# Kernel optimization log

Hardware: AMD Instinct MI355X
Metric: run time of the kernel (lower is better)

Reference implementation:

```python
import jax, jax.numpy as jnp
import numpy as np

B, NL, C, H, W = 4, 2048, 128, 128, 128
N_PTS0, N_PTS1 = 32, 8
SCALE = N_PTS0 // N_PTS1  # MaxPool1d kernel/stride
FEATURE_DIM = 5
BN_EPS = 1e-5


def setup_inputs() -> dict:
    key = jax.random.key(0)
    ks = jax.random.split(key, 12)
    fm = jax.random.normal(ks[0], (B, C, H, W), dtype=jnp.float32)
    lines = jax.random.uniform(ks[1], (B, NL, 2, 2), dtype=jnp.float32) * 128.0
    P = C // 2
    s = 0.05
    return {
        "feature_map": fm,
        "lines": lines,
        # Bottleneck1D params (BatchNorm in eval mode: running_mean=0, running_var=1)
        "bn1_g": jnp.ones((C,), jnp.float32), "bn1_b": jnp.zeros((C,), jnp.float32),
        "conv1_w": jax.random.normal(ks[2], (P, C, 1), jnp.float32) * s,
        "conv1_b": jnp.zeros((P,), jnp.float32),
        "bn2_g": jnp.ones((P,), jnp.float32), "bn2_b": jnp.zeros((P,), jnp.float32),
        "conv2_w": jax.random.normal(ks[3], (P, P, 3), jnp.float32) * s,
        "conv2_b": jnp.zeros((P,), jnp.float32),
        "bn3_g": jnp.ones((P,), jnp.float32), "bn3_b": jnp.zeros((P,), jnp.float32),
        "conv3_w": jax.random.normal(ks[4], (C, P, 1), jnp.float32) * s,
        "conv3_b": jnp.zeros((C,), jnp.float32),
        # fc2: ReLU -> Linear(dim_loi*n_pts1 + 5, 4)
        "fc2_w": jax.random.normal(ks[5], (4, C * N_PTS1 + FEATURE_DIM), jnp.float32) * s,
        "fc2_b": jnp.zeros((4,), jnp.float32),
    }


def _bn(x, g, b):
    # eval-mode BatchNorm1d with running_mean=0, running_var=1
    return x * (g / jnp.sqrt(1.0 + BN_EPS))[None, :, None] + b[None, :, None]


def _conv1d(x, w, b, pad):
    y = jax.lax.conv_general_dilated(x, w, (1,), [(pad, pad)],
                                     dimension_numbers=("NCH", "OIH", "NCH"))
    return y + b[None, :, None]


def _loi_gather(fm, lines):
    # sample points along each line: [B, NL, N_PTS0, 2]
    lam = jnp.linspace(0.0, 1.0, N_PTS0, dtype=jnp.float32)[None, None, :, None]
    p = lines[:, :, 0:1, :] * lam + lines[:, :, 1:2, :] * (1.0 - lam) - 0.5
    p = p.reshape(B, -1, 2)                      # [B, NL*N_PTS0, 2]
    px, py = p[..., 0], p[..., 1]
    px0 = jnp.clip(jnp.floor(px), 0.0, 127.0)
    py0 = jnp.clip(jnp.floor(py), 0.0, 127.0)
    px1 = jnp.clip(px0 + 1.0, 0.0, 127.0)
    py1 = jnp.clip(py0 + 1.0, 0.0, 127.0)
    px0l, py0l = px0.astype(jnp.int32), py0.astype(jnp.int32)
    px1l, py1l = px1.astype(jnp.int32), py1.astype(jnp.int32)

    gather = jax.vmap(lambda f, yi, xi: f[:, yi, xi])  # [C, P] per image
    # weights exactly as in the torch source
    xp = (gather(fm, py0l, px0l) * ((px1 - px) * (py1 - py))[:, None, :]
          + gather(fm, py1l, px0l) * ((px - px0) * (py1 - py))[:, None, :]
          + gather(fm, py0l, px1l) * ((px1 - px) * (py - py0))[:, None, :]
          + gather(fm, py1l, px1l) * ((px - px0) * (py - py0))[:, None, :])
    # [B, C, NL*N_PTS0] -> [B*NL, C, N_PTS0]
    xp = xp.reshape(B, C, NL, N_PTS0).transpose(0, 2, 1, 3).reshape(B * NL, C, N_PTS0)
    return xp


def reference(feature_map, lines, bn1_g, bn1_b, conv1_w, conv1_b,
              bn2_g, bn2_b, conv2_w, conv2_b, bn3_g, bn3_b,
              conv3_w, conv3_b, fc2_w, fc2_b):
    xp = _loi_gather(feature_map, lines)               # [B*NL, C, N_PTS0]
    # MaxPool1d(SCALE, SCALE)
    x = xp.reshape(B * NL, C, N_PTS1, SCALE).max(axis=-1)
    # Bottleneck1D residual block
    y = jax.nn.relu(_bn(x, bn1_g, bn1_b))
    y = _conv1d(y, conv1_w, conv1_b, 0)
    y = jax.nn.relu(_bn(y, bn2_g, bn2_b))
    y = _conv1d(y, conv2_w, conv2_b, 1)
    y = jax.nn.relu(_bn(y, bn3_g, bn3_b))
    y = _conv1d(y, conv3_w, conv3_b, 0)
    x = x + y                                          # [B*NL, C, N_PTS1]
    # line geometry feature (use_cood=1, use_slop=1)
    xyu, xyv = lines[:, :, 0, :], lines[:, :, 1, :]
    u2v = jnp.sqrt(((xyu - xyv) ** 2).sum(-1, keepdims=True)).clip(min=1e-6)
    f = jnp.concatenate([xyu / 128.0, xyv / 128.0, u2v], axis=-1)
    f = f.reshape(B * NL, FEATURE_DIM)
    # concat + fc2 (ReLU -> Linear)
    x = jnp.concatenate([x.reshape(B * NL, C * N_PTS1), f], axis=1)
    logits = jax.nn.relu(x) @ fc2_w.T + fc2_b
    prob = jax.nn.softmax(logits, axis=1)
    return logits, prob
```

## Files before the change

### kernel.cpp

```cpp
#include <hip/hip_runtime.h>
#include <math.h>

#define BB 4
#define NLL 2048
#define CC 128
#define HH 128
#define WW 128
#define NPTS0 32
#define NPTS1 8
#define PP 64
#define FDIM 5
#define FCK (CC*NPTS1 + FDIM)
#define FCKP 1032

typedef __attribute__((ext_vector_type(8))) short bf16x8;
typedef __attribute__((ext_vector_type(4))) float f32x4;

__device__ __forceinline__ unsigned short f2bf(float f) {
    union { float f; unsigned u; } v; v.f = f;
    unsigned u = v.u;
    return (unsigned short)((u + 0x7fffu + ((u >> 16) & 1u)) >> 16);
}
__device__ __forceinline__ float bf2f(unsigned short s) {
    union { unsigned u; float f; } v; v.u = ((unsigned)s) << 16;
    return v.f;
}

__global__ __launch_bounds__(256)
void transpose_prep(const float* __restrict__ fm, const float* __restrict__ w1,
                    const float* __restrict__ w2, const float* __restrict__ w3,
                    const float* __restrict__ fcw,
                    unsigned short* __restrict__ fmT,
                    unsigned short* __restrict__ W1b,
                    unsigned short* __restrict__ W2b,
                    unsigned short* __restrict__ W3b,
                    float* __restrict__ fcwP) {
    const int t = threadIdx.x;
    if (blockIdx.x >= 1024) {
        int gid = (blockIdx.x - 1024) * 256 + t;
        for (int e = gid; e < 32800; e += 4096) {
            if (e < 8192) {
                W1b[e] = f2bf(w1[e]);
            } else if (e < 20480) {
                int g = e - 8192;
                int tt = g >> 12, r = g & 4095;
                int p = r >> 6, q = r & 63;
                W2b[tt * 4096 + p * 64 + q] = f2bf(w2[p * 192 + q * 3 + tt]);
            } else if (e < 28672) {
                int g = e - 20480;
                W3b[g] = f2bf(w3[g]);
            } else {
                int g = e - 28672;
                int o = g / FCKP, r = g - o * FCKP;
                fcwP[g] = (r < FCK) ? fcw[o * FCK + r] : 0.0f;
            }
        }
        return;
    }
    __shared__ unsigned short tile[128 * 72];
    const int bh = blockIdx.x;
    const int by = bh >> 1;
    const int h  = bh & 1;
    const int b = by >> 7, y = by & 127;
    const float* src = fm + ((size_t)b * CC) * (HH * WW) + (size_t)y * WW + h * 64;
    const int x4 = (t & 15) * 4;
    #pragma unroll
    for (int i = 0; i < 8; ++i) {
        int r = (t >> 4) + 16 * i;
        float4 v = *(const float4*)&src[(size_t)r * (HH * WW) + x4];
        ushort4 u;
        u.x = f2bf(v.x); u.y = f2bf(v.y); u.z = f2bf(v.z); u.w = f2bf(v.w);
        *(ushort4*)&tile[r * 72 + (x4 ^ (r & 28))] = u;
    }
    __syncthreads();
    const int c4 = (t & 31) * 4;
    unsigned short* dst = fmT + ((size_t)by * WW + h * 64) * CC;
    #pragma unroll
    for (int i = 0; i < 8; ++i) {
        int x = (t >> 5) + 8 * i;
        ushort4 u;
        u.x = tile[(c4 + 0) * 72 + (x ^ ((c4 + 0) & 28))];
        u.y = tile[(c4 + 1) * 72 + (x ^ ((c4 + 1) & 28))];
        u.z = tile[(c4 + 2) * 72 + (x ^ ((c4 + 2) & 28))];
        u.w = tile[(c4 + 3) * 72 + (x ^ ((c4 + 3) & 28))];
        *(ushort4*)&dst[(size_t)x * CC + c4] = u;
    }
}

__global__ __launch_bounds__(256, 5)
void line_mfma(const unsigned short* __restrict__ fmT,
               const float* __restrict__ lines,
               const float* __restrict__ bn1_g, const float* __restrict__ bn1_b,
               const unsigned short* __restrict__ W1b, const float* __restrict__ b1,
               const float* __restrict__ bn2_g, const float* __restrict__ bn2_b,
               const unsigned short* __restrict__ W2b, const float* __restrict__ b2,
               const float* __restrict__ bn3_g, const float* __restrict__ bn3_b,
               const unsigned short* __restrict__ W3b, const float* __restrict__ b3,
               const float* __restrict__ fcwP,  const float* __restrict__ fcb,
               float* __restrict__ out) {
    __shared__ int   s_oA[64], s_oB[64], s_oC[64], s_oD[64];
    __shared__ float s_wA[64], s_wB[64], s_wC[64], s_wD[64];
    __shared__ float s_xs[16 * 132];
    __shared__ unsigned short s_ybn[16 * 136];
    __shared__ unsigned short s_z1[2 * 10 * 72];
    __shared__ unsigned short s_z2[16 * 72];
    __shared__ float s_feat[2][8];
    __shared__ float s_red[4 * 8];

    const int bx  = blockIdx.x;
    const int L0  = bx * 2;
    const int b   = bx >> 10;
    const int tid = threadIdx.x;
    const int lane = tid & 63;
    const int wv   = tid >> 6;
    const int quad = lane >> 4;
    const int l16  = lane & 15;
    const float inv_s = 1.0f / sqrtf(1.0f + 1e-5f);

    if (tid < 64) {
        int line = tid >> 5, pt = tid & 31;
        const float* ln = lines + (size_t)(L0 + line) * 4;
        float lam = (float)pt * (1.0f / 31.0f);
        float om  = 1.0f - lam;
        float px = ln[0] * lam + ln[2] * om - 0.5f;
        float py = ln[1] * lam + ln[3] * om - 0.5f;
        float px0 = fminf(fmaxf(floorf(px), 0.0f), 127.0f);
        float py0 = fminf(fmaxf(floorf(py), 0.0f), 127.0f);
        float px1 = fminf(px0 + 1.0f, 127.0f);
        float py1 = fminf(py0 + 1.0f, 127.0f);
        int ix0 = (int)px0, ix1 = (int)px1, iy0 = (int)py0, iy1 = (int)py1;
        s_oA[tid] = (iy0 * WW + ix0) * CC;
        s_oB[tid] = (iy1 * WW + ix0) * CC;
        s_oC[tid] = (iy0 * WW + ix1) * CC;
        s_oD[tid] = (iy1 * WW + ix1) * CC;
        float ax = px1 - px, bxv = px - px0, ay = py1 - py, byv = py - py0;
        s_wA[tid] = ax  * ay;
        s_wB[tid] = bxv * ay;
        s_wC[tid] = ax  * byv;
        s_wD[tid] = bxv * byv;
    }
    if (tid >= 64 && tid < 66) {
        int line = tid - 64;
        const float* ln = lines + (size_t)(L0 + line) * 4;
        float ux = ln[0], uy = ln[1], vx = ln[2], vy = ln[3];
        float dx = ux - vx, dy = uy - vy;
        float d = fmaxf(sqrtf(dx * dx + dy * dy), 1e-6f);
        s_feat[line][0] = ux * (1.0f / 128.0f);
        s_feat[line][1] = uy * (1.0f / 128.0f);
        s_feat[line][2] = vx * (1.0f / 128.0f);
        s_feat[line][3] = vy * (1.0f / 128.0f);
        s_feat[line][4] = d;
    }
    if (tid < 128) {
        int line = tid >> 6, q = tid & 63;
        s_z1[line * 720 + 0 * 72 + q] = 0;
        s_z1[line * 720 + 9 * 72 + q] = 0;
    }
    __syncthreads();

    {
        int tl = tid >> 4;
        int line = tl >> 3, k = tl & 7;
        int c8 = (tid & 15) * 8;
        const unsigned short* base = fmT + (size_t)b * (HH * WW * CC) + c8;
        const int pt0 = line * 32 + k * 4;
        bf16x8 rA[4], rB[4], rC[4], rD[4];
        #pragma unroll
        for (int j = 0; j < 4; ++j) {
            rA[j] = *(const bf16x8*)(base + s_oA[pt0 + j]);
            rB[j] = *(const bf16x8*)(base + s_oB[pt0 + j]);
            rC[j] = *(const bf16x8*)(base + s_oC[pt0 + j]);
            rD[j] = *(const bf16x8*)(base + s_oD[pt0 + j]);
        }
        float acc[8];
        #pragma unroll
        for (int i = 0; i < 8; ++i) acc[i] = -INFINITY;
        #pragma unroll
        for (int j = 0; j < 4; ++j) {
            int pt = pt0 + j;
            float wA = s_wA[pt], wB = s_wB[pt], wC = s_wC[pt], wD = s_wD[pt];
            #pragma unroll
            for (int i = 0; i < 8; ++i) {
                float v = wA * bf2f((unsigned short)rA[j][i])
                        + wB * bf2f((unsigned short)rB[j][i])
                        + wC * bf2f((unsigned short)rC[j][i])
                        + wD * bf2f((unsigned short)rD[j][i]);
                acc[i] = fmaxf(acc[i], v);
            }
        }
        float* xr = &s_xs[tl * 132 + c8];
        f32x4 lo = {acc[0], acc[1], acc[2], acc[3]};
        f32x4 hi = {acc[4], acc[5], acc[6], acc[7]};
        *(f32x4*)&xr[0] = lo;
        *(f32x4*)&xr[4] = hi;
        bf16x8 pack;
        #pragma unroll
        for (int i = 0; i < 8; ++i) {
            float v = fmaxf(acc[i] * (bn1_g[c8 + i] * inv_s) + bn1_b[c8 + i], 0.0f);
            pack[i] = (short)f2bf(v);
        }
        *(bf16x8*)&s_ybn[tl * 136 + c8] = pack;
    }
    __syncthreads();

    {
        int n0 = wv * 16;
        f32x4 acc = {0.f, 0.f, 0.f, 0.f};
        #pragma unroll
        for (int kc = 0; kc < 4; ++kc) {
            bf16x8 a = *(const bf16x8*)&s_ybn[l16 * 136 + kc * 32 + quad * 8];
            bf16x8 bf = *(const bf16x8*)(W1b + (n0 + l16) * 128 + kc * 32 + quad * 8);
            acc = __builtin_amdgcn_mfma_f32_16x16x32_bf16(a, bf, acc, 0, 0, 0);
        }
        int p = n0 + l16;
        float s2 = bn2_g[p] * inv_s, bb2 = bn2_b[p], cb = b1[p];
        int line = quad >> 1;
        int kbase = (quad & 1) * 4;
        #pragma unroll
        for (int r = 0; r < 4; ++r) {
            float v = fmaxf((acc[r] + cb) * s2 + bb2, 0.0f);
            s_z1[line * 720 + (kbase + r + 1) * 72 + p] = f2bf(v);
        }
    }
    __syncthreads();

    {
        int n0 = wv * 16;
        f32x4 acc = {0.f, 0.f, 0.f, 0.f};
        int line = l16 >> 3, k = l16 & 7;
        #pragma unroll
        for (int t = 0; t < 3; ++t) {
            const unsigned short* arow = &s_z1[line * 720 + (k + t) * 72];
            #pragma unroll
            for (int kc = 0; kc < 2; ++kc) {
                bf16x8 a = *(const bf16x8*)&arow[kc * 32 + quad * 8];
                bf16x8 bf = *(const bf16x8*)(W2b + t * 4096 + (n0 + l16) * 64 + kc * 32 + quad * 8);
                acc = __builtin_amdgcn_mfma_f32_16x16x32_bf16(a, bf, acc, 0, 0, 0);
            }
        }
        int p = n0 + l16;
        float s3 = bn3_g[p] * inv_s, bb3 = bn3_b[p], cb = b2[p];
        #pragma unroll
        for (int r = 0; r < 4; ++r) {
            float v = fmaxf((acc[r] + cb) * s3 + bb3, 0.0f);
            s_z2[(quad * 4 + r) * 72 + p] = f2bf(v);
        }
    }
    __syncthreads();

    float p0 = 0.f, p1 = 0.f, p2 = 0.f, p3 = 0.f;
    {
        int kbase = (quad & 1) * 4;
        bf16x8 a0 = *(const bf16x8*)&s_z2[l16 * 72 + 0 * 32 + quad * 8];
        bf16x8 a1 = *(const bf16x8*)&s_z2[l16 * 72 + 1 * 32 + quad * 8];
        #pragma unroll
        for (int sub = 0; sub < 2; ++sub) {
            int n0 = wv * 32 + sub * 16;
            f32x4 acc = {0.f, 0.f, 0.f, 0.f};
            bf16x8 bf0 = *(const bf16x8*)(W3b + (n0 + l16) * 64 + 0 * 32 + quad * 8);
            bf16x8 bf1 = *(const bf16x8*)(W3b + (n0 + l16) * 64 + 1 * 32 + quad * 8);
            acc = __builtin_amdgcn_mfma_f32_16x16x32_bf16(a0, bf0, acc, 0, 0, 0);
            acc = __builtin_amdgcn_mfma_f32_16x16x32_bf16(a1, bf1, acc, 0, 0, 0);
            int c = n0 + l16;
            float cb = b3[c];
            int idx = c * 8 + kbase;
            float4 w0 = *(const float4*)(fcwP + 0 * FCKP + idx);
            float4 w1v = *(const float4*)(fcwP + 1 * FCKP + idx);
            float4 w2v = *(const float4*)(fcwP + 2 * FCKP + idx);
            float4 w3v = *(const float4*)(fcwP + 3 * FCKP + idx);
            const float* w0a = (const float*)&w0;
            const float* w1a = (const float*)&w1v;
            const float* w2a = (const float*)&w2v;
            const float* w3a = (const float*)&w3v;
            #pragma unroll
            for (int r = 0; r < 4; ++r) {
                int m = quad * 4 + r;
                float v = fmaxf(s_xs[m * 132 + c] + acc[r] + cb, 0.0f);
                p0 = fmaf(v, w0a[r], p0);
                p1 = fmaf(v, w1a[r], p1);
                p2 = fmaf(v, w2a[r], p2);
                p3 = fmaf(v, w3a[r], p3);
            }
        }
    }
    #pragma unroll
    for (int off = 16; off >= 1; off >>= 1) {
        p0 += __shfl_down(p0, off);
        p1 += __shfl_down(p1, off);
        p2 += __shfl_down(p2, off);
        p3 += __shfl_down(p3, off);
    }
    if ((lane & 31) == 0) {
        int line = lane >> 5;
        s_red[wv * 8 + line * 4 + 0] = p0;
        s_red[wv * 8 + line * 4 + 1] = p1;
        s_red[wv * 8 + line * 4 + 2] = p2;
        s_red[wv * 8 + line * 4 + 3] = p3;
    }
    __syncthreads();

    if (tid < 2) {
        int line = tid;
        float lg[4];
        #pragma unroll
        for (int o = 0; o < 4; ++o) {
            lg[o] = fcb[o] + s_red[0 + line * 4 + o] + s_red[8 + line * 4 + o]
                  + s_red[16 + line * 4 + o] + s_red[24 + line * 4 + o];
        }
        #pragma unroll
        for (int j = 0; j < FDIM; ++j) {
            float fv = fmaxf(s_feat[line][j], 0.0f);
            #pragma unroll
            for (int o = 0; o < 4; ++o)
                lg[o] = fmaf(fv, fcwP[o * FCKP + 1024 + j], lg[o]);
        }
        float m = fmaxf(fmaxf(lg[0], lg[1]), fmaxf(lg[2], lg[3]));
        float e0 = expf(lg[0] - m), e1 = expf(lg[1] - m);
        float e2 = expf(lg[2] - m), e3 = expf(lg[3] - m);
        float inv = 1.0f / (e0 + e1 + e2 + e3);
        float* lo = out + (size_t)(L0 + line) * 4;
        lo[0] = lg[0]; lo[1] = lg[1]; lo[2] = lg[2]; lo[3] = lg[3];
        float* pr = out + (size_t)BB * NLL * 4 + (size_t)(L0 + line) * 4;
        pr[0] = e0 * inv; pr[1] = e1 * inv; pr[2] = e2 * inv; pr[3] = e3 * inv;
    }
}

__global__ __launch_bounds__(256)
void transpose_fm2(const float* __restrict__ fm, float* __restrict__ fmT) {
    __shared__ float tile[32 * 132];
    const int c0 = blockIdx.x * 32;
    const int by = blockIdx.y;
    const int b = by >> 7, y = by & 127;
    const int t = threadIdx.x;
    const float* src = fm + ((size_t)b * CC) * (HH * WW) + (size_t)y * WW;
    const int x4 = (t & 31) * 4;
    #pragma unroll
    for (int i = 0; i < 4; ++i) {
        int r = (t >> 5) + 8 * i;
        *(float4*)&tile[r * 132 + x4] =
            *(const float4*)&src[(size_t)(c0 + r) * (HH * WW) + x4];
    }
    __syncthreads();
    float* dst = fmT + (size_t)by * WW * CC + c0 + (t & 31);
    const int cr = (t & 31) * 132;
    #pragma unroll
    for (int i = 0; i < 16; ++i) {
        int x = (t >> 5) + 8 * i;
        dst[(size_t)x * CC] = tile[cr + x];
    }
}

template<bool TRANS>
__global__ __launch_bounds__(256)
void line_kernel_v1(const float* __restrict__ fm,
                    const float* __restrict__ lines,
                    const float* __restrict__ bn1_g, const float* __restrict__ bn1_b,
                    const float* __restrict__ w1,    const float* __restrict__ b1,
                    const float* __restrict__ bn2_g, const float* __restrict__ bn2_b,
                    const float* __restrict__ w2,    const float* __restrict__ b2,
                    const float* __restrict__ bn3_g, const float* __restrict__ bn3_b,
                    const float* __restrict__ w3,    const float* __restrict__ b3,
                    const float* __restrict__ fcw,   const float* __restrict__ fcb,
                    float* __restrict__ out) {
    __shared__ int   s_ix0[32], s_ix1[32], s_iy0[32], s_iy1[32];
    __shared__ float s_wA[32], s_wB[32], s_wC[32], s_wD[32];
    __shared__ float xs [8][132];
    __shared__ float ybn[8][132];
    __shared__ float z1 [64][12];
    __shared__ float z2 [64][8];
    __shared__ float s_feat[8];
    __shared__ float s_red[16];

    const int L   = blockIdx.x;
    const int b   = L / NLL;
    const int tid = threadIdx.x;
    const float inv_s = 1.0f / sqrtf(1.0f + 1e-5f);
    const float* ln = lines + (size_t)L * 4;

    if (tid < 32) {
        float lam = (float)tid * (1.0f / 31.0f);
        float om  = 1.0f - lam;
        float px = ln[0] * lam + ln[2] * om - 0.5f;
        float py = ln[1] * lam + ln[3] * om - 0.5f;
        float px0 = fminf(fmaxf(floorf(px), 0.0f), 127.0f);
        float py0 = fminf(fmaxf(floorf(py), 0.0f), 127.0f);
        float px1 = fminf(px0 + 1.0f, 127.0f);
        float py1 = fminf(py0 + 1.0f, 127.0f);
        s_ix0[tid] = (int)px0; s_ix1[tid] = (int)px1;
        s_iy0[tid] = (int)py0; s_iy1[tid] = (int)py1;
        float ax = px1 - px, bxv = px - px0, ay = py1 - py, byv = py - py0;
        s_wA[tid] = ax  * ay;  s_wB[tid] = bxv * ay;
        s_wC[tid] = ax  * byv; s_wD[tid] = bxv * byv;
    }
    if (tid == 0) {
        float ux = ln[0], uy = ln[1], vx = ln[2], vy = ln[3];
        float dx = ux - vx, dy = uy - vy;
        float d = fmaxf(sqrtf(dx * dx + dy * dy), 1e-6f);
        s_feat[0] = ux / 128.0f; s_feat[1] = uy / 128.0f;
        s_feat[2] = vx / 128.0f; s_feat[3] = vy / 128.0f;
        s_feat[4] = d;
    }
    __syncthreads();
    {
        int cq = tid & 31, k = tid >> 5, c0 = cq * 4;
        float4 acc;
        acc.x = -INFINITY; acc.y = -INFINITY; acc.z = -INFINITY; acc.w = -INFINITY;
        #pragma unroll
        for (int j = 0; j < 4; ++j) {
            int pt = k * 4 + j;
            int ix0 = s_ix0[pt], ix1 = s_ix1[pt];
            int iy0 = s_iy0[pt], iy1 = s_iy1[pt];
            float wA = s_wA[pt], wB = s_wB[pt], wC = s_wC[pt], wD = s_wD[pt];
            float4 vA, vB, vC, vD;
            if (TRANS) {
                const float* base = fm + (size_t)b * HH * WW * CC;
                vA = *(const float4*)(base + ((size_t)(iy0 * WW + ix0)) * CC + c0);
                vB = *(const float4*)(base + ((size_t)(iy1 * WW + ix0)) * CC + c0);
                vC = *(const float4*)(base + ((size_t)(iy0 * WW + ix1)) * CC + c0);
                vD = *(const float4*)(base + ((size_t)(iy1 * WW + ix1)) * CC + c0);
            } else {
                const float* base = fm + ((size_t)b * CC + c0) * HH * WW;
                int oA = iy0 * WW + ix0, oB = iy1 * WW + ix0;
                int oC = iy0 * WW + ix1, oD = iy1 * WW + ix1;
                vA.x = base[oA];           vB.x = base[oB];
                vC.x = base[oC];           vD.x = base[oD];
                vA.y = base[HH*WW + oA];   vB.y = base[HH*WW + oB];
                vC.y = base[HH*WW + oC];   vD.y = base[HH*WW + oD];
                vA.z = base[2*HH*WW + oA]; vB.z = base[2*HH*WW + oB];
                vC.z = base[2*HH*WW + oC]; vD.z = base[2*HH*WW + oD];
                vA.w = base[3*HH*WW + oA]; vB.w = base[3*HH*WW + oB];
                vC.w = base[3*HH*WW + oC]; vD.w = base[3*HH*WW + oD];
            }
            float4 v;
            v.x = wA * vA.x + wB * vB.x + wC * vC.x + wD * vD.x;
            v.y = wA * vA.y + wB * vB.y + wC * vC.y + wD * vD.y;
            v.z = wA * vA.z + wB * vB.z + wC * vC.z + wD * vD.z;
            v.w = wA * vA.w + wB * vB.w + wC * vC.w + wD * vD.w;
            acc.x = fmaxf(acc.x, v.x); acc.y = fmaxf(acc.y, v.y);
            acc.z = fmaxf(acc.z, v.z); acc.w = fmaxf(acc.w, v.w);
        }
        *(float4*)(&xs[k][c0]) = acc;
    }
    __syncthreads();
    for (int e = tid; e < 1024; e += 256) {
        int k = e >> 7, c = e & 127;
        ybn[k][c] = fmaxf(xs[k][c] * (bn1_g[c] * inv_s) + bn1_b[c], 0.0f);
    }
    __syncthreads();
    if (tid < 64) { z1[tid][0] = 0.0f; z1[tid][9] = 0.0f; }
    {
        int p = tid >> 2, kq = tid & 3;
        const float* wrow = w1 + p * 128;
        float a0a = 0.f, a0b = 0.f, a1a = 0.f, a1b = 0.f;
        #pragma unroll 8
        for (int c = 0; c < 128; c += 4) {
            float4 w  = *(const float4*)(wrow + c);
            float4 ya = *(const float4*)(&ybn[kq][c]);
            float4 yb = *(const float4*)(&ybn[kq + 4][c]);
            a0a = fmaf(w.x, ya.x, a0a); a0b = fmaf(w.y, ya.y, a0b);
            a0a = fmaf(w.z, ya.z, a0a); a0b = fmaf(w.w, ya.w, a0b);
            a1a = fmaf(w.x, yb.x, a1a); a1b = fmaf(w.y, yb.y, a1b);
            a1a = fmaf(w.z, yb.z, a1a); a1b = fmaf(w.w, yb.w, a1b);
        }
        float s2 = bn2_g[p] * inv_s, bb = bn2_b[p], cb = b1[p];
        z1[p][1 + kq]     = fmaxf((a0a + a0b + cb) * s2 + bb, 0.0f);
        z1[p][1 + kq + 4] = fmaxf((a1a + a1b + cb) * s2 + bb, 0.0f);
    }
    __syncthreads();
    {
        int p = tid >> 2, kq = tid & 3;
        const float* wrow = w2 + p * 192;
        float acc0 = 0.f, acc1 = 0.f;
        #pragma unroll 4
        for (int q = 0; q < 64; ++q) {
            float w0 = wrow[q * 3 + 0], w1v = wrow[q * 3 + 1], w2v = wrow[q * 3 + 2];
            const float* zr = &z1[q][0];
            acc0 = fmaf(w0, zr[kq], acc0);
            acc0 = fmaf(w1v, zr[kq + 1], acc0);
            acc0 = fmaf(w2v, zr[kq + 2], acc0);
            acc1 = fmaf(w0, zr[kq + 4], acc1);
            acc1 = fmaf(w1v, zr[kq + 5], acc1);
            acc1 = fmaf(w2v, zr[kq + 6], acc1);
        }
        float s3 = bn3_g[p] * inv_s, bb = bn3_b[p], cb = b2[p];
        z2[p][kq]     = fmaxf((acc0 + cb) * s3 + bb, 0.0f);
        z2[p][kq + 4] = fmaxf((acc1 + cb) * s3 + bb, 0.0f);
    }
    __syncthreads();
    float part0 = 0.f, part1 = 0.f, part2 = 0.f, part3 = 0.f;
    {
        int c = tid >> 1, kq = tid & 1;
        const float* wrow = w3 + c * 64;
        float acc[4] = {0.f, 0.f, 0.f, 0.f};
        #pragma unroll 8
        for (int q = 0; q < 64; ++q) {
            float w = wrow[q];
            acc[0] = fmaf(w, z2[q][kq], acc[0]);
            acc[1] = fmaf(w, z2[q][kq + 2], acc[1]);
            acc[2] = fmaf(w, z2[q][kq + 4], acc[2]);
            acc[3] = fmaf(w, z2[q][kq + 6], acc[3]);
        }
        float cb = b3[c];
        #pragma unroll
        for (int i = 0; i < 4; ++i) {
            int k = kq + 2 * i;
            float v = fmaxf(xs[k][c] + acc[i] + cb, 0.0f);
            int idx = c * 8 + k;
            part0 = fmaf(v, fcw[0 * FCK + idx], part0);
            part1 = fmaf(v, fcw[1 * FCK + idx], part1);
            part2 = fmaf(v, fcw[2 * FCK + idx], part2);
            part3 = fmaf(v, fcw[3 * FCK + idx], part3);
        }
    }
    #pragma unroll
    for (int off = 32; off > 0; off >>= 1) {
        part0 += __shfl_down(part0, off);
        part1 += __shfl_down(part1, off);
        part2 += __shfl_down(part2, off);
        part3 += __shfl_down(part3, off);
    }
    if ((tid & 63) == 0) {
        int w = tid >> 6;
        s_red[w * 4 + 0] = part0; s_red[w * 4 + 1] = part1;
        s_red[w * 4 + 2] = part2; s_red[w * 4 + 3] = part3;
    }
    __syncthreads();
    if (tid == 0) {
        float lg[4];
        #pragma unroll
        for (int o = 0; o < 4; ++o)
            lg[o] = fcb[o] + s_red[o] + s_red[4 + o] + s_red[8 + o] + s_red[12 + o];
        #pragma unroll
        for (int j = 0; j < FDIM; ++j) {
            float fv = fmaxf(s_feat[j], 0.0f);
            #pragma unroll
            for (int o = 0; o < 4; ++o)
                lg[o] = fmaf(fv, fcw[o * FCK + 1024 + j], lg[o]);
        }
        float m = fmaxf(fmaxf(lg[0], lg[1]), fmaxf(lg[2], lg[3]));
        float e0 = expf(lg[0] - m), e1 = expf(lg[1] - m);
        float e2 = expf(lg[2] - m), e3 = expf(lg[3] - m);
        float inv = 1.0f / (e0 + e1 + e2 + e3);
        float* lo = out + (size_t)L * 4;
        lo[0] = lg[0]; lo[1] = lg[1]; lo[2] = lg[2]; lo[3] = lg[3];
        float* pr = out + (size_t)BB * NLL * 4 + (size_t)L * 4;
        pr[0] = e0 * inv; pr[1] = e1 * inv; pr[2] = e2 * inv; pr[3] = e3 * inv;
    }
}

extern "C" void kernel_launch(void* const* d_in, const int* in_sizes, int n_in,
                              void* d_out, int out_size, void* d_ws, size_t ws_size,
                              hipStream_t stream) {
    const float* fm     = (const float*)d_in[0];
    const float* lines  = (const float*)d_in[1];
    const float* bn1_g  = (const float*)d_in[2];
    const float* bn1_b  = (const float*)d_in[3];
    const float* w1     = (const float*)d_in[4];
    const float* b1     = (const float*)d_in[5];
    const float* bn2_g  = (const float*)d_in[6];
    const float* bn2_b  = (const float*)d_in[7];
    const float* w2     = (const float*)d_in[8];
    const float* b2     = (const float*)d_in[9];
    const float* bn3_g  = (const float*)d_in[10];
    const float* bn3_b  = (const float*)d_in[11];
    const float* w3     = (const float*)d_in[12];
    const float* b3     = (const float*)d_in[13];
    const float* fcw    = (const float*)d_in[14];
    const float* fcb    = (const float*)d_in[15];
    float* out = (float*)d_out;

    const size_t fmTb_bytes = (size_t)BB * HH * WW * CC * sizeof(unsigned short);
    const size_t fmTf_bytes = (size_t)BB * HH * WW * CC * sizeof(float);
    const size_t wb_bytes   = 57344;
    const size_t fcwP_bytes = 4 * FCKP * sizeof(float);

    if (ws_size >= fmTb_bytes + wb_bytes + fcwP_bytes) {
        unsigned short* fmT = (unsigned short*)d_ws;
        unsigned short* W1b = (unsigned short*)((char*)d_ws + fmTb_bytes);
        unsigned short* W2b = W1b + 8192;
        unsigned short* W3b = W2b + 12288;
        float* fcwP = (float*)((char*)d_ws + fmTb_bytes + wb_bytes);
        transpose_prep<<<1024 + 16, 256, 0, stream>>>(
            fm, w1, w2, w3, fcw, fmT, W1b, W2b, W3b, fcwP);
        line_mfma<<<BB * NLL / 2, 256, 0, stream>>>(
            fmT, lines, bn1_g, bn1_b, W1b, b1, bn2_g, bn2_b, W2b, b2,
            bn3_g, bn3_b, W3b, b3, fcwP, fcb, out);
    } else if (ws_size >= fmTf_bytes) {
        float* fmT = (float*)d_ws;
        dim3 tg(CC / 32, BB * HH);
        transpose_fm2<<<tg, 256, 0, stream>>>(fm, fmT);
        line_kernel_v1<true><<<BB * NLL, 256, 0, stream>>>(
            fmT, lines, bn1_g, bn1_b, w1, b1, bn2_g, bn2_b, w2, b2,
            bn3_g, bn3_b, w3, b3, fcw, fcb, out);
    } else {
        line_kernel_v1<false><<<BB * NLL, 256, 0, stream>>>(
            fm, lines, bn1_g, bn1_b, w1, b1, bn2_g, bn2_b, w2, b2,
            bn3_g, bn3_b, w3, b3, fcw, fcb, out);
    }
}
```

Before: 152.2 us.

## Process four lines per 512-thread block with swizzled block-to-line mapping

Each workgroup of line_mfma now handles four lines with 512 threads (two 16-row M tiles across eight waves) instead of two lines with 256 threads. Block indices are also permuted so that consecutive block IDs spread across batch regions, which changes the order in which feature-map rows are touched by concurrently running blocks. The aim is to amortise per-block setup and weight fetches over more lines and to improve cache locality across XCDs. The cost is a larger shared-memory footprint per block and a tighter launch bound (512 threads, 8 waves per EU), which can force register spills.

New measurement: 191.6 us. 1.26x slower.

```diff
diff --git a/kernel.cpp b/kernel.cpp
--- a/kernel.cpp
+++ b/kernel.cpp
@@ -87,7 +87,7 @@
     }
 }
 
-__global__ __launch_bounds__(256, 5)
+__global__ __launch_bounds__(512, 8)
 void line_mfma(const unsigned short* __restrict__ fmT,
                const float* __restrict__ lines,
                const float* __restrict__ bn1_g, const float* __restrict__ bn1_b,
@@ -98,26 +98,29 @@
                const unsigned short* __restrict__ W3b, const float* __restrict__ b3,
                const float* __restrict__ fcwP,  const float* __restrict__ fcb,
                float* __restrict__ out) {
-    __shared__ int   s_oA[64], s_oB[64], s_oC[64], s_oD[64];
-    __shared__ float s_wA[64], s_wB[64], s_wC[64], s_wD[64];
-    __shared__ float s_xs[16 * 132];
-    __shared__ unsigned short s_ybn[16 * 136];
-    __shared__ unsigned short s_z1[2 * 10 * 72];
-    __shared__ unsigned short s_z2[16 * 72];
-    __shared__ float s_feat[2][8];
-    __shared__ float s_red[4 * 8];
+    __shared__ int   s_oA[128], s_oB[128], s_oC[128], s_oD[128];
+    __shared__ float s_wA[128], s_wB[128], s_wC[128], s_wD[128];
+    __shared__ float s_xs[32 * 132];
+    __shared__ unsigned short s_ybn[32 * 136];
+    __shared__ unsigned short s_z1[4 * 10 * 72];
+    __shared__ unsigned short s_z2[32 * 72];
+    __shared__ float s_feat[4][8];
+    __shared__ float s_red[8 * 8];
 
     const int bx  = blockIdx.x;
-    const int L0  = bx * 2;
-    const int b   = bx >> 10;
+    const int wg  = (bx & 7) * 256 + (bx >> 3);
+    const int L0  = wg * 4;
+    const int b   = wg >> 9;
     const int tid = threadIdx.x;
     const int lane = tid & 63;
     const int wv   = tid >> 6;
+    const int mt   = wv >> 2;
+    const int wn   = wv & 3;
     const int quad = lane >> 4;
     const int l16  = lane & 15;
     const float inv_s = 1.0f / sqrtf(1.0f + 1e-5f);
 
-    if (tid < 64) {
+    if (tid < 128) {
         int line = tid >> 5, pt = tid & 31;
         const float* ln = lines + (size_t)(L0 + line) * 4;
         float lam = (float)pt * (1.0f / 31.0f);
@@ -139,8 +142,8 @@
         s_wC[tid] = ax  * byv;
         s_wD[tid] = bxv * byv;
     }
-    if (tid >= 64 && tid < 66) {
-        int line = tid - 64;
+    if (tid >= 128 && tid < 132) {
+        int line = tid - 128;
         const float* ln = lines + (size_t)(L0 + line) * 4;
         float ux = ln[0], uy = ln[1], vx = ln[2], vy = ln[3];
         float dx = ux - vx, dy = uy - vy;
@@ -151,10 +154,9 @@
         s_feat[line][3] = vy * (1.0f / 128.0f);
         s_feat[line][4] = d;
     }
-    if (tid < 128) {
-        int line = tid >> 6, q = tid & 63;
-        s_z1[line * 720 + 0 * 72 + q] = 0;
-        s_z1[line * 720 + 9 * 72 + q] = 0;
+    {
+        int line = tid >> 7, rr = (tid >> 6) & 1, q = tid & 63;
+        s_z1[line * 720 + rr * 648 + q] = 0;
     }
     __syncthreads();
 
@@ -204,17 +206,17 @@
     __syncthreads();
 
     {
-        int n0 = wv * 16;
+        int n0 = wn * 16;
         f32x4 acc = {0.f, 0.f, 0.f, 0.f};
         #pragma unroll
         for (int kc = 0; kc < 4; ++kc) {
-            bf16x8 a = *(const bf16x8*)&s_ybn[l16 * 136 + kc * 32 + quad * 8];
+            bf16x8 a = *(const bf16x8*)&s_ybn[(mt * 16 + l16) * 136 + kc * 32 + quad * 8];
             bf16x8 bf = *(const bf16x8*)(W1b + (n0 + l16) * 128 + kc * 32 + quad * 8);
             acc = __builtin_amdgcn_mfma_f32_16x16x32_bf16(a, bf, acc, 0, 0, 0);
         }
         int p = n0 + l16;
         float s2 = bn2_g[p] * inv_s, bb2 = bn2_b[p], cb = b1[p];
-        int line = quad >> 1;
+        int line = mt * 2 + (quad >> 1);
         int kbase = (quad & 1) * 4;
         #pragma unroll
         for (int r = 0; r < 4; ++r) {
@@ -225,12 +227,12 @@
     __syncthreads();
 
     {
-        int n0 = wv * 16;
+        int n0 = wn * 16;
         f32x4 acc = {0.f, 0.f, 0.f, 0.f};
-        int line = l16 >> 3, k = l16 & 7;
+        int aline = mt * 2 + (l16 >> 3), k = l16 & 7;
         #pragma unroll
         for (int t = 0; t < 3; ++t) {
-            const unsigned short* arow = &s_z1[line * 720 + (k + t) * 72];
+            const unsigned short* arow = &s_z1[aline * 720 + (k + t) * 72];
             #pragma unroll
             for (int kc = 0; kc < 2; ++kc) {
                 bf16x8 a = *(const bf16x8*)&arow[kc * 32 + quad * 8];
@@ -243,7 +245,7 @@
         #pragma unroll
         for (int r = 0; r < 4; ++r) {
             float v = fmaxf((acc[r] + cb) * s3 + bb3, 0.0f);
-            s_z2[(quad * 4 + r) * 72 + p] = f2bf(v);
+            s_z2[(mt * 16 + quad * 4 + r) * 72 + p] = f2bf(v);
         }
     }
     __syncthreads();
@@ -251,11 +253,11 @@
     float p0 = 0.f, p1 = 0.f, p2 = 0.f, p3 = 0.f;
     {
         int kbase = (quad & 1) * 4;
-        bf16x8 a0 = *(const bf16x8*)&s_z2[l16 * 72 + 0 * 32 + quad * 8];
-        bf16x8 a1 = *(const bf16x8*)&s_z2[l16 * 72 + 1 * 32 + quad * 8];
+        bf16x8 a0 = *(const bf16x8*)&s_z2[(mt * 16 + l16) * 72 + 0 * 32 + quad * 8];
+        bf16x8 a1 = *(const bf16x8*)&s_z2[(mt * 16 + l16) * 72 + 1 * 32 + quad * 8];
         #pragma unroll
         for (int sub = 0; sub < 2; ++sub) {
-            int n0 = wv * 32 + sub * 16;
+            int n0 = wn * 32 + sub * 16;
             f32x4 acc = {0.f, 0.f, 0.f, 0.f};
             bf16x8 bf0 = *(const bf16x8*)(W3b + (n0 + l16) * 64 + 0 * 32 + quad * 8);
             bf16x8 bf1 = *(const bf16x8*)(W3b + (n0 + l16) * 64 + 1 * 32 + quad * 8);
@@ -274,7 +276,7 @@
             const float* w3a = (const float*)&w3v;
             #pragma unroll
             for (int r = 0; r < 4; ++r) {
-                int m = quad * 4 + r;
+                int m = mt * 16 + quad * 4 + r;
                 float v = fmaxf(s_xs[m * 132 + c] + acc[r] + cb, 0.0f);
                 p0 = fmaf(v, w0a[r], p0);
                 p1 = fmaf(v, w1a[r], p1);
@@ -291,21 +293,25 @@
         p3 += __shfl_down(p3, off);
     }
     if ((lane & 31) == 0) {
-        int line = lane >> 5;
-        s_red[wv * 8 + line * 4 + 0] = p0;
-        s_red[wv * 8 + line * 4 + 1] = p1;
-        s_red[wv * 8 + line * 4 + 2] = p2;
-        s_red[wv * 8 + line * 4 + 3] = p3;
-    }
-    __syncthreads();
-
-    if (tid < 2) {
+        int half = lane >> 5;
+        s_red[wv * 8 + half * 4 + 0] = p0;
+        s_red[wv * 8 + half * 4 + 1] = p1;
+        s_red[wv * 8 + half * 4 + 2] = p2;
+        s_red[wv * 8 + half * 4 + 3] = p3;
+    }
+    __syncthreads();
+
+    if (tid < 4) {
         int line = tid;
+        int mtl = line >> 1, half = line & 1;
         float lg[4];
         #pragma unroll
         for (int o = 0; o < 4; ++o) {
-            lg[o] = fcb[o] + s_red[0 + line * 4 + o] + s_red[8 + line * 4 + o]
-                  + s_red[16 + line * 4 + o] + s_red[24 + line * 4 + o];
+            float s = fcb[o];
+            #pragma unroll
+            for (int j = 0; j < 4; ++j)
+                s += s_red[(mtl * 4 + j) * 8 + half * 4 + o];
+            lg[o] = s;
         }
         #pragma unroll
         for (int j = 0; j < FDIM; ++j) {
@@ -582,7 +588,7 @@
         float* fcwP = (float*)((char*)d_ws + fmTb_bytes + wb_bytes);
         transpose_prep<<<1024 + 16, 256, 0, stream>>>(
             fm, w1, w2, w3, fcw, fmT, W1b, W2b, W3b, fcwP);
-        line_mfma<<<BB * NLL / 2, 256, 0, stream>>>(
+        line_mfma<<<BB * NLL / 4, 512, 0, stream>>>(
             fmT, lines, bn1_g, bn1_b, W1b, b1, bn2_g, bn2_b, W2b, b2,
             bn3_g, bn3_b, W3b, b3, fcwP, fcb, out);
     } else if (ws_size >= fmTf_bytes) {
```
